# Optimization experiments

Hardware: AMD Instinct MI355X
Metric: run time of the kernel (lower is better)

## Reference

```python
import jax, jax.numpy as jnp
import numpy as np

B, C, H, W = 16, 1, 512, 512
D, F, KH, KW = 4, 24, 5, 5   # numWienerFilters, output_features, reg-filter size
BKH, BKW = 9, 9              # blur kernel size
LB, UB = 1e-4, 1e-2


def psf2otf(psf, shape):
    # zero-pad psf to `shape`, circularly shift its center to (0,0), FFT
    kh, kw = psf.shape[-2], psf.shape[-1]
    pad = [(0, 0)] * (psf.ndim - 2) + [(0, shape[0] - kh), (0, shape[1] - kw)]
    p = jnp.pad(psf, pad)
    p = jnp.roll(p, shift=(-((kh - 1) // 2), -((kw - 1) // 2)), axis=(-2, -1))
    return jnp.fft.fft2(p)


def _taper_profile(proj, n):
    # autocorrelation of the psf projection, periodized to length n (MATLAB edgetaper)
    z = jnp.zeros(n - 1, proj.dtype).at[: proj.shape[0]].set(proj)
    zf = jnp.fft.fft(z)
    acf = jnp.real(jnp.fft.ifft(zf * jnp.conj(zf)))
    acf = jnp.concatenate([acf, acf[:1]])
    return acf / acf.max()


def _normalize_weights(w, scale):
    # WeightNormalization5D: zero-mean + L2-normalize over (C,kh,kw), times scale
    w = w - w.mean(axis=(2, 3, 4), keepdims=True)
    nrm = jnp.sqrt(jnp.sum(w * w, axis=(2, 3, 4), keepdims=True))
    return w * (scale[..., None, None, None] / nrm)


def setup_inputs():
    key = jax.random.key(0)
    ks = jax.random.split(key, 4)
    x = jax.random.uniform(ks[0], (B, C, H, W), jnp.float32)
    bk = jax.random.uniform(ks[1], (BKH, BKW), jnp.float32) + 1e-3
    bk = bk / bk.sum()  # normalized blur PSF
    stdn = jax.random.uniform(ks[2], (B,), jnp.float32) * 0.1 + 0.01
    conv_weights = jax.random.normal(ks[3], (D, F, C, KH, KW), jnp.float32)
    scale = jnp.full((D, F), 0.1, jnp.float32)
    alpha = jnp.log(jnp.logspace(np.log10(LB), np.log10(UB), D))[:, None].astype(jnp.float32)
    return {"x": x, "blur_kernel": bk, "stdn": stdn,
            "conv_weights": conv_weights, "scale": scale, "alpha": alpha}


def reference(x, blur_kernel, stdn, conv_weights, scale, alpha):
    kh, kw = blur_kernel.shape
    # getPad2RetainShape
    pt, pb = (kh + 1) // 2 - 1, kh - (kh + 1) // 2
    pl, pr = (kw + 1) // 2 - 1, kw - (kw + 1) // 2
    xp = jnp.pad(x, ((0, 0), (0, 0), (pt, pb), (pl, pr)), mode="symmetric")
    Hp, Wp = xp.shape[-2], xp.shape[-1]
    otf = psf2otf(blur_kernel, (Hp, Wp))                     # (Hp,Wp) complex
    # EdgeTaper: blend image with its circular blur near borders
    br = _taper_profile(blur_kernel.sum(axis=1), Hp)
    bc = _taper_profile(blur_kernel.sum(axis=0), Wp)
    taper = (1.0 - br)[:, None] * (1.0 - bc)[None, :]
    blurred = jnp.real(jnp.fft.ifft2(jnp.fft.fft2(xp) * otf))
    xp = taper * xp + (1.0 - taper) * blurred
    # regularization-filter OTFs
    w = _normalize_weights(conv_weights, scale)              # (D,F,C,kh,kw)
    G = psf2otf(w, (Hp, Wp))                                 # (D,F,C,Hp,Wp)
    S = jnp.sum(G.real ** 2 + G.imag ** 2, axis=1)           # (D,C,Hp,Wp)
    a = jnp.exp(alpha)[:, :, None, None]                     # (D,1,1,1)
    B2 = otf.real ** 2 + otf.imag ** 2                       # (Hp,Wp)
    denom = B2[None, None] + a * S                           # (D,C,Hp,Wp)
    Y = jnp.conj(otf) * jnp.fft.fft2(xp)                     # (B,C,Hp,Wp)
    Xf = Y[:, None] / denom[None]                            # (B,D,C,Hp,Wp)
    out = jnp.real(jnp.fft.ifft2(Xf))[..., pt:Hp - pb, pl:Wp - pr]
    # colored-noise std factor per (wiener filter, channel)
    cvar = jnp.mean(B2[None, None] / denom ** 2, axis=(-2, -1))   # (D,C)
    cvar = jnp.broadcast_to(cvar[None], (x.shape[0],) + cvar.shape)  # (B,D,C)
    cstdn = jnp.sqrt(stdn[:, None] ** 2 * cvar.mean(axis=2))        # (B,D)
    return out, cstdn
```

## Files before the change

kernel.cpp:

```cpp
#include <hip/hip_runtime.h>
#include <math.h>

#define NP    520
#define NN    (520*520)
#define HH    512
#define NPIX  (512*512)
#define NB    16
#define NPAIR 8
#define ND    4
#define NF    24
#define KS    544
#define RS    576
#define PLANE ((size_t)RS*KS)
#define S8P   (8*PLANE)
#define E9SZ  (NP*9)
#define CSZ   (ND*9*NP)
#define NBORD 18396
#define PADCH 5536
#define TWO_PI 6.283185307179586f

typedef unsigned short u16;
typedef __attribute__((ext_vector_type(8))) short bf16x8;
typedef __attribute__((ext_vector_type(4))) float f32x4;

__device__ __forceinline__ int wrap520(int t){ t %= NP; return t < 0 ? t + NP : t; }

__device__ __forceinline__ u16 f2bf(float f){
  unsigned u = __float_as_uint(f);
  u += 0x7FFFu + ((u >> 16) & 1u);
  return (u16)(u >> 16);
}
__device__ __forceinline__ float bf2f(u16 h){
  return __uint_as_float(((unsigned)h) << 16);
}
__device__ __forceinline__ void gll16(const u16* g, u16* l){
  __builtin_amdgcn_global_load_lds(
      (const __attribute__((address_space(1))) void*)g,
      (__attribute__((address_space(3))) void*)l, 16, 0, 0);
}
template<int N> __device__ __forceinline__ void vmwait(){
  if constexpr (N == 0)       asm volatile("s_waitcnt vmcnt(0)" ::: "memory");
  else if constexpr (N == 4)  asm volatile("s_waitcnt vmcnt(4)" ::: "memory");
  else if constexpr (N == 6)  asm volatile("s_waitcnt vmcnt(6)" ::: "memory");
  else if constexpr (N == 8)  asm volatile("s_waitcnt vmcnt(8)" ::: "memory");
  else if constexpr (N == 12) asm volatile("s_waitcnt vmcnt(12)" ::: "memory");
}
#define MF(a,b,c) __builtin_amdgcn_mfma_f32_16x16x32_bf16((a),(b),(c),0,0,0)


__global__ __launch_bounds__(256) void zwb_k(u16* __restrict__ slabs, int nSlices,
                                             u16* __restrict__ wf, u16* __restrict__ wi){
  int idx = blockIdx.x*256 + threadIdx.x;
  int nA = nSlices*PADCH;
  if (idx < nA){
    int pl = idx / PADCH, cc = idx % PADCH;
    int row, col;
    if (cc < 1728){ row = cc/3; col = 520 + (cc%3)*8; }
    else { int c2 = cc - 1728; row = 520 + c2/68; col = (c2%68)*8; }
    bf16x8 z = {0,0,0,0,0,0,0,0};
    *(bf16x8*)(slabs + (size_t)pl*PLANE + (size_t)row*KS + col) = z;
    return;
  }
  idx -= nA;
  if (idx >= (int)PLANE) return;
  int r = idx / KS, k = idx % KS;
  float fr=0.f, fi=0.f, ir=0.f, ii=0.f;
  if (r < NP && k < NP){
    int m = (int)(((long long)r * (long long)k) % NP);
    float ang = TWO_PI * (float)m / (float)NP;
    float s, c; sincosf(ang, &s, &c);
    fr = c; fi = -s;
    ir = c * (1.0f/NP); ii = s * (1.0f/NP);
  }
  wf[0*PLANE+idx] = f2bf(fr); wf[1*PLANE+idx] = f2bf(fi);
  wi[0*PLANE+idx] = f2bf(ir); wi[1*PLANE+idx] = f2bf(ii);
}

__global__ __launch_bounds__(256) void setup1_k(const float* __restrict__ bk,
                                                const float* __restrict__ cw,
                                                const float* __restrict__ scale,
                                                float* __restrict__ e9,
                                                float* __restrict__ r_row, float* __restrict__ r_col,
                                                float* __restrict__ wn){
  int idx = blockIdx.x*256 + threadIdx.x;
  if (idx < NP*9){
    int u = idx / 9, t = idx % 9;
    int m = wrap520(u*(t-4));
    float ang = TWO_PI * (float)m / (float)NP;
    float s, c; sincosf(ang, &s, &c);
    e9[idx] = c; e9[E9SZ + idx] = -s;
    return;
  }
  idx -= NP*9;
  if (idx < 18){
    int k = idx % 9;
    bool rowp = (idx < 9);
    float proj[9];
    for (int m = 0; m < 9; ++m){
      float a = 0.f;
      for (int j = 0; j < 9; ++j) a += rowp ? bk[m*9+j] : bk[j*9+m];
      proj[m] = a;
    }
    float acc = 0.f;
    for (int m = 0; m + k < 9; ++m) acc += proj[m] * proj[m+k];
    (rowp ? r_row : r_col)[k] = acc;
    return;
  }
  idx -= 18;
  if (idx >= ND*NF) return;
  const float* wp = cw + idx*25;
  float mean = 0.f;
  for (int k = 0; k < 25; ++k) mean += wp[k];
  mean *= (1.0f/25.0f);
  float ss = 0.f;
  for (int k = 0; k < 25; ++k){ float d = wp[k]-mean; ss += d*d; }
  float sc = scale[idx] / sqrtf(ss);
  for (int k = 0; k < 25; ++k) wn[idx*25+k] = (wp[k]-mean)*sc;
}

__global__ __launch_bounds__(256) void setup2_k(const float* __restrict__ bk,
                                                const float* __restrict__ e9,
                                                const float* __restrict__ wn,
                                                float* __restrict__ T, float* __restrict__ R){
  int idx = blockIdx.x*256 + threadIdx.x;
  if (idx < 9*NP){
    int i = idx / NP, v = idx % NP;
    float tr = 0.f, ti = 0.f;
    #pragma unroll
    for (int j = 0; j < 9; ++j){
      float w = bk[i*9+j];
      tr += w * e9[v*9+j];
      ti += w * e9[E9SZ + v*9+j];
    }
    T[idx] = tr; T[9*NP + idx] = ti;
    return;
  }
  idx -= 9*NP;
  if (idx >= ND*81) return;
  int d = idx / 81, t = idx % 81;
  int di = t/9 - 4, dj = t%9 - 4;
  int i0 = di > 0 ? di : 0, i1 = di < 0 ? 4+di : 4;
  int j0 = dj > 0 ? dj : 0, j1 = dj < 0 ? 4+dj : 4;
  float acc = 0.f;
  for (int f = 0; f < NF; ++f){
    const float* w = wn + (d*NF+f)*25;
    for (int i = i0; i <= i1; ++i)
      for (int j = j0; j <= j1; ++j)
        acc += w[i*5+j] * w[(i-di)*5 + (j-dj)];
  }
  R[idx] = acc;
}

__global__ void C_k(const float* __restrict__ R, const float* __restrict__ e9,
                    float* __restrict__ Ctab){
  int idx = blockIdx.x*blockDim.x + threadIdx.x;
  if (idx >= ND*9*NP) return;
  int v = idx % NP, t9 = idx / NP;
  int d = t9 / 9, t = t9 % 9;
  float cr = 0.f, ci = 0.f;
  #pragma unroll
  for (int s = 0; s < 9; ++s){
    float r = R[d*81 + t*9 + s];
    cr += r * e9[v*9+s];
    ci += r * e9[E9SZ + v*9+s];
  }
  Ctab[idx] = cr; Ctab[CSZ + idx] = ci;
}

__global__ __launch_bounds__(256) void denomMT2_k(
    const float* __restrict__ Tb, const float* __restrict__ e9,
    const float* __restrict__ Ctab, const float* __restrict__ alpha,
    float* __restrict__ MTre, float* __restrict__ MTim, float* __restrict__ cvar){
  __shared__ float red[256];
  const int d = blockIdx.y;
  const int p = blockIdx.x*256 + threadIdx.x;
  float contrib = 0.f;
  if (p < NN){
    int u = p % NP, v = p / NP;
    float ar = 0.f, ai = 0.f;
    #pragma unroll
    for (int i = 0; i < 9; ++i){
      float er = e9[u*9+i], ei = e9[E9SZ + u*9+i];
      float tr = Tb[i*NP+v], ti = Tb[9*NP + i*NP+v];
      ar += er*tr - ei*ti;
      ai += er*ti + ei*tr;
    }
    float S = 0.f;
    #pragma unroll
    for (int t = 0; t < 9; ++t){
      float er = e9[u*9+t], ei = e9[E9SZ + u*9+t];
      float cr = Ctab[(d*9+t)*NP + v], ci = Ctab[CSZ + (d*9+t)*NP + v];
      S += er*cr - ei*ci;
    }
    float B2 = ar*ar + ai*ai;
    size_t idx = (size_t)d*NN + p;
    float dv = B2 + expf(alpha[d]) * S;
    MTre[idx] = ar / dv;
    MTim[idx] = -ai / dv;
    contrib = B2 / (dv*dv);
  }
  red[threadIdx.x] = contrib; __syncthreads();
  for (int s = 128; s > 0; s >>= 1){
    if (threadIdx.x < s) red[threadIdx.x] += red[threadIdx.x+s];
    __syncthreads();
  }
  if (threadIdx.x == 0) atomicAdd(&cvar[d], red[0]);
}

__global__ void cstdn_k(const float* __restrict__ stdn, const float* __restrict__ cvar,
                        float* __restrict__ out){
  int t = threadIdx.x;
  if (t >= NB*ND) return;
  int b = t >> 2, d = t & 3;
  float s = stdn[b];
  out[(size_t)NB*ND*NPIX + t] = sqrtf(s*s*cvar[d]*(1.0f/(float)NN));
}

__global__ __launch_bounds__(256) void pad_tr_k(const float* __restrict__ x,
                                                u16* __restrict__ MA){
  __shared__ float tile[64][65];
  const int q  = blockIdx.z;
  const int r0 = blockIdx.y * 64;
  const int c0 = blockIdx.x * 64;
  const int t  = threadIdx.x;
  const float* xq = x + (size_t)q*NPIX;
  const int jl = t & 63, ib = t >> 6;
  const bool fast = (c0 >= 64 && c0 <= 448 && r0 >= 64 && r0 <= 448);

  if (fast){
    #pragma unroll 1
    for (int pass = 0; pass < 16; ++pass){
      int il = ib + pass*4;
      tile[il][jl] = xq[(size_t)(c0+il-4)*HH + (r0+jl-4)];
    }
  } else {
    #pragma unroll 1
    for (int pass = 0; pass < 16; ++pass){
      int il = ib + pass*4;
      int I = c0 + il, J = r0 + jl;
      float v = 0.f;
      if (I < NP && J < NP){
        int si = I - 4; si = (si < 0) ? (-si-1) : ((si >= HH) ? (2*HH-1-si) : si);
        int sj = J - 4; sj = (sj < 0) ? (-sj-1) : ((sj >= HH) ? (2*HH-1-sj) : sj);
        v = xq[(size_t)si*HH + sj];
      }
      tile[il][jl] = v;
    }
  }
  __syncthreads();

  const int cchunk = t & 7, rb = t >> 3;
  const int pair = q >> 1, pl = q & 1;
  #pragma unroll
  for (int half = 0; half < 2; ++half){
    int rl = rb + half*32;
    int r = r0 + rl, cg = c0 + cchunk*8;
    if (r >= NP || cg >= NP) continue;
    bf16x8 vh;
    #pragma unroll
    for (int e = 0; e < 8; ++e)
      vh[e] = (short)f2bf(tile[cchunk*8+e][rl]);
    size_t o = (size_t)pair*PLANE + (size_t)r*KS + cg;
    *(bf16x8*)(MA + (size_t)pl*S8P + o) = vh;
  }
}

__global__ __launch_bounds__(256) void border_k(const float* __restrict__ x,
                                                const float* __restrict__ bk,
                                                const float* __restrict__ r_row,
                                                const float* __restrict__ r_col,
                                                u16* __restrict__ MA){
  __shared__ float bks[81], rr_[9], rc_[9];
  if (threadIdx.x < 81) bks[threadIdx.x] = bk[threadIdx.x];
  if (threadIdx.x < 9){ rr_[threadIdx.x] = r_row[threadIdx.x]; rc_[threadIdx.x] = r_col[threadIdx.x]; }
  __syncthreads();
  int idx = blockIdx.x*256 + threadIdx.x;
  if (idx >= NB*NBORD) return;
  int q = idx / NBORD, t = idx % NBORD;
  int I, J;
  if (t < 9360){ int ri = t / 520; I = (ri < 9) ? ri : 502 + ri; J = t % 520; }
  else { int s = t - 9360; I = 9 + s / 18; int ci = s % 18; J = (ci < 9) ? ci : 502 + ci; }
  const float* xq = x + (size_t)q*NPIX;
  auto XP = [&](int ii, int jj)->float{
    int si = ii - 4; si = (si < 0) ? (-si-1) : ((si >= HH) ? (2*HH-1-si) : si);
    int sj = jj - 4; sj = (sj < 0) ? (-sj-1) : ((sj >= HH) ? (2*HH-1-sj) : sj);
    return xq[(size_t)si*HH + sj];
  };
  float v = XP(I, J);
  float brv = (I < 9) ? rr_[I] : ((I >= 511) ? rr_[519-I] : 0.f);
  float bcv = (J < 9) ? rc_[J] : ((J >= 511) ? rc_[519-J] : 0.f);
  brv /= rr_[0]; bcv /= rc_[0];
  float tp = (1.f - brv) * (1.f - bcv);
  float blur = 0.f;
  for (int a = 0; a < 9; ++a){
    int ii = wrap520(I - a + 4);
    for (int b2 = 0; b2 < 9; ++b2){
      int jj = wrap520(J - b2 + 4);
      blur += bks[a*9+b2] * XP(ii, jj);
    }
  }
  v = tp*v + (1.f - tp)*blur;
  int pair = q >> 1, pl = q & 1;
  MA[(size_t)pl*S8P + (size_t)pair*PLANE + (size_t)J*KS + I] = f2bf(v);
}

__global__ __launch_bounds__(256) void maskF_k(const u16* __restrict__ IN, u16* __restrict__ OUT,
                                               const float* __restrict__ Mre, const float* __restrict__ Mim){
  int idx = blockIdx.x*256 + threadIdx.x;
  if (idx >= NPAIR*NP*65) return;
  int pr = idx / (NP*65), rem = idx % (NP*65);
  int r = rem / 65, c0 = (rem % 65)*8;
  size_t o = (size_t)pr*PLANE + (size_t)r*KS + c0;
  bf16x8 qr = *(const bf16x8*)(IN + 0*S8P + o);
  bf16x8 qi = *(const bf16x8*)(IN + 1*S8P + o);
  const float* mrp = Mre + (size_t)r*NP + c0;
  const float* mip = Mim + (size_t)r*NP + c0;
  bf16x8 o0, o1;
  #pragma unroll
  for (int e = 0; e < 8; ++e){
    float vr = bf2f((u16)qr[e]), vi = bf2f((u16)qi[e]);
    float mr = mrp[e], mi = mip[e];
    o0[e] = (short)f2bf(vr*mr - vi*mi);
    o1[e] = (short)f2bf(vr*mi + vi*mr);
  }
  *(bf16x8*)(OUT + 0*S8P + o) = o0;
  *(bf16x8*)(OUT + 1*S8P + o) = o1;
}

template<int BM, int CROP, int MASKOUT>
__global__ __launch_bounds__(256) void gemm_k(
    const u16* __restrict__ P, size_t pPl, size_t pZp, size_t pZd,
    const u16* __restrict__ Q, size_t qPl, size_t qZp, size_t qZd,
    u16* __restrict__ O, size_t oPl, size_t oZp, size_t oZd,
    float* __restrict__ cropOut, int dBase,
    const float* __restrict__ Mre, const float* __restrict__ Mim)
{
  constexpr int NW = 4;
  constexpr int FR = BM/32;
  constexpr int TR = BM/16;
  constexpr int LPW = 4*TR/NW;
  constexpr int PLSTR = BM*32;
  constexpr int BUF = 4*PLSTR;
  constexpr int NK = KS/32;
  __shared__ u16 lds[3*BUF];
  const int tid = threadIdx.x;
  const int l = tid & 63, w = tid >> 6;

  const int gx = gridDim.x, gy = gridDim.y;
  int lin = blockIdx.x + gx*(blockIdx.y + gy*blockIdx.z);
  int ntot = gx*gy*gridDim.z;
  int q8 = ntot >> 3, r8 = ntot & 7;
  int xcd = lin & 7, id8 = lin >> 3;
  int nl = (xcd < r8 ? xcd*(q8+1) : r8*(q8+1) + (xcd-r8)*q8) + id8;
  int BX = nl % gx; int t2 = nl / gx;
  int BY = t2 % gy; int BZ = t2 / gy;

  const int pair = BZ & 7;
  const int dd = dBase + (BZ >> 3);
  const int R0 = BY * BM, C0 = BX * BM;

  const u16* Pb = P + (size_t)pair*pZp + (size_t)dd*pZd;
  const u16* Qb = Q + (size_t)pair*qZp + (size_t)dd*qZd;

  const int s = l >> 2;
  const int cs8 = ((l & 3) ^ ((s >> 1) & 3)) * 8;
  const size_t pOff0 = (size_t)(R0 + s)*KS + cs8;
  const size_t qOff0 = (size_t)(C0 + s)*KS + cs8;

  const int lm = l & 15, lc = l >> 4;
  const int wm = w >> 1, wn = w & 1;

  f32x4 zero4 = {0.f, 0.f, 0.f, 0.f};
  f32x4 aRe[FR][FR], aIm[FR][FR];
  #pragma unroll
  for (int i = 0; i < FR; ++i)
    #pragma unroll
    for (int j = 0; j < FR; ++j){ aRe[i][j] = zero4; aIm[i][j] = zero4; }

  auto STAGE = [&](int bi, int k0){
    u16* dst = lds + bi*BUF;
    #pragma unroll
    for (int i = 0; i < LPW; ++i){
      int t = w + i*NW;
      int q2 = t / TR, r2 = t % TR;
      const u16* src = (q2 < 2) ? (Pb + (size_t)q2*pPl + pOff0)
                                : (Qb + (size_t)(q2-2)*qPl + qOff0);
      gll16(src + (size_t)(r2*16)*KS + k0, dst + q2*PLSTR + r2*512);
    }
  };

  STAGE(0, 0);
  STAGE(1, 32);

  #pragma unroll 1
  for (int kt = 0; kt < NK; ++kt){
    if (kt + 2 < NK) STAGE((kt+2)%3, (kt+2)*32);
    if (kt + 2 < NK)      vmwait<2*LPW>();
    else if (kt + 1 < NK) vmwait<LPW>();
    else                  vmwait<0>();
    __builtin_amdgcn_sched_barrier(0);
    __builtin_amdgcn_s_barrier();
    __builtin_amdgcn_sched_barrier(0);

    const u16* buf = lds + (kt%3)*BUF;
    bf16x8 pf[FR][2];
    #pragma unroll
    for (int mi = 0; mi < FR; ++mi){
      int r = wm*(FR*16) + mi*16 + lm;
      int co = ((lc ^ ((r >> 1) & 3)) << 3);
      pf[mi][0] = *(const bf16x8*)(buf + 0*PLSTR + r*32 + co);
      pf[mi][1] = *(const bf16x8*)(buf + 1*PLSTR + r*32 + co);
    }
    #pragma unroll
    for (int ni = 0; ni < FR; ++ni){
      int r = wn*(FR*16) + ni*16 + lm;
      int co = ((lc ^ ((r >> 1) & 3)) << 3);
      bf16x8 q0 = *(const bf16x8*)(buf + 2*PLSTR + r*32 + co);
      bf16x8 q1 = *(const bf16x8*)(buf + 3*PLSTR + r*32 + co);
      #pragma unroll
      for (int mi = 0; mi < FR; ++mi){
        bf16x8 nw = pf[mi][1] ^ (short)0x8000;
        f32x4 re = aRe[mi][ni], im = aIm[mi][ni];
        re = MF(pf[mi][0], q0, re);
        re = MF(nw,        q1, re);
        im = MF(pf[mi][0], q1, im);
        im = MF(pf[mi][1], q0, im);
        aRe[mi][ni] = re; aIm[mi][ni] = im;
      }
    }
    __builtin_amdgcn_sched_barrier(0);
    __builtin_amdgcn_s_barrier();
    __builtin_amdgcn_sched_barrier(0);
  }

  u16* Ob = O ? (O + (size_t)pair*oZp + (size_t)dd*oZd) : nullptr;
  #pragma unroll
  for (int mi = 0; mi < FR; ++mi)
    #pragma unroll
    for (int ni = 0; ni < FR; ++ni){
      int cb = C0 + wn*(FR*16) + ni*16 + lm;
      int rb = R0 + wm*(FR*16) + mi*16 + lc*4;
      #pragma unroll
      for (int e = 0; e < 4; ++e){
        int rr = rb + e;
        float vr = aRe[mi][ni][e], vi = aIm[mi][ni][e];
        if (CROP){
          if (rr >= 4 && rr < 516 && cb >= 4 && cb < 516){
            size_t px = (size_t)(rr-4)*HH + (cb-4);
            cropOut[((size_t)(2*pair  )*ND + dd)*NPIX + px] = vr;
            cropOut[((size_t)(2*pair+1)*ND + dd)*NPIX + px] = vi;
          }
        } else if (MASKOUT){
          if (rr < NP && cb < NP){
            size_t o = (size_t)rr*KS + cb;
            size_t mo = (size_t)rr*NP + cb;
            #pragma unroll
            for (int d2 = 0; d2 < ND; ++d2){
              float mr = Mre[(size_t)d2*NN + mo], mi2 = Mim[(size_t)d2*NN + mo];
              u16* Od = O + (size_t)d2*oZd + (size_t)pair*oZp;
              Od[0*oPl+o] = f2bf(vr*mr - vi*mi2);
              Od[1*oPl+o] = f2bf(vr*mi2 + vi*mr);
            }
          }
        } else {
          if (rr < NP && cb < NP){
            size_t o = (size_t)rr*KS + cb;
            Ob[0*oPl+o] = f2bf(vr);
            Ob[1*oPl+o] = f2bf(vi);
          }
        }
      }
    }
}


extern "C" void kernel_launch(void* const* d_in, const int* in_sizes, int n_in,
                              void* d_out, int out_size, void* d_ws, size_t ws_size,
                              hipStream_t stream){
  const float* x     = (const float*)d_in[0];
  const float* bk    = (const float*)d_in[1];
  const float* stdn  = (const float*)d_in[2];
  const float* cw    = (const float*)d_in[3];
  const float* scale = (const float*)d_in[4];
  const float* alpha = (const float*)d_in[5];
  float* out = (float*)d_out;

  char* base = (char*)d_ws;
  const size_t UNIT = 16*PLANE*sizeof(u16);
  size_t off;
  auto alloc = [&](size_t bytes)->void*{
    void* p = base + off;
    off += (bytes + 255) & ~(size_t)255;
    return p;
  };

  u16 *MA, *MB, *MC, *Dm, *Do, *WF, *WI;
  float *MTre, *MTim, *e9, *Tb, *Rarr, *Ctab, *r_row, *r_col, *wn, *cvar;
  auto layout = [&](bool bigL){
    off = 0;
    MA = (u16*)alloc(UNIT);
    MB = (u16*)alloc(UNIT);
    if (bigL){ Dm = (u16*)alloc(4*UNIT); Do = (u16*)alloc(4*UNIT); MC = nullptr; }
    else     { MC = (u16*)alloc(UNIT);   Dm = nullptr; Do = nullptr; }
    WF = (u16*)alloc(2*PLANE*sizeof(u16));
    WI = (u16*)alloc(2*PLANE*sizeof(u16));
    MTre = (float*)alloc((size_t)ND*NN*4);
    MTim = (float*)alloc((size_t)ND*NN*4);
    e9   = (float*)alloc(2*E9SZ*4);
    Tb   = (float*)alloc(2*9*NP*4);
    Rarr = (float*)alloc(ND*81*4);
    Ctab = (float*)alloc(2*CSZ*4);
    r_row = (float*)alloc(64);
    r_col = (float*)alloc(64);
    wn   = (float*)alloc(ND*NF*25*4);
    cvar = (float*)alloc(64);
    return off;
  };
  bool big = (layout(true) <= ws_size);
  if (!big){
    if (layout(false) > ws_size) return;
  }

  hipMemsetAsync(cvar, 0, ND*sizeof(float), stream);

  const int nSlices = big ? 160 : 48;
  {
    int ztot = nSlices*PADCH + (int)PLANE;
    zwb_k<<<(ztot+255)/256, 256, 0, stream>>>(MA, nSlices, WF, WI);
  }
  setup1_k<<<(NP*9+18+ND*NF+255)/256, 256, 0, stream>>>(bk, cw, scale, e9, r_row, r_col, wn);
  setup2_k<<<(9*NP+ND*81+255)/256, 256, 0, stream>>>(bk, e9, wn, Tb, Rarr);
  C_k     <<<(ND*9*NP+255)/256, 256, 0, stream>>>(Rarr, e9, Ctab);
  {
    dim3 gd((NN+255)/256, ND);
    denomMT2_k<<<gd, 256, 0, stream>>>(Tb, e9, Ctab, alpha, MTre, MTim, cvar);
  }
  cstdn_k <<<1, 64, 0, stream>>>(stdn, cvar, out);
  pad_tr_k<<<dim3(9, 9, NB), 256, 0, stream>>>(x, MA);
  border_k<<<(NB*NBORD+255)/256, 256, 0, stream>>>(x, bk, r_row, r_col, MA);

  gemm_k<64,0,0><<<dim3(9,9,8),256,0,stream>>>(
      WF, PLANE, 0, 0,   MA, S8P, PLANE, 0,   MB, S8P, PLANE, 0,
      nullptr, 0, nullptr, nullptr);

  if (big){
    gemm_k<64,0,1><<<dim3(9,9,8),256,0,stream>>>(
        WF, PLANE, 0, 0,   MB, S8P, PLANE, 0,   Dm, S8P, PLANE, 16*PLANE,
        nullptr, 0, MTre, MTim);
    gemm_k<96,0,0><<<dim3(6,6,32),256,0,stream>>>(
        WI, PLANE, 0, 0,   Dm, S8P, PLANE, 16*PLANE,   Do, S8P, PLANE, 16*PLANE,
        nullptr, 0, nullptr, nullptr);
    gemm_k<96,1,0><<<dim3(6,6,32),256,0,stream>>>(
        Do, S8P, PLANE, 16*PLANE,   WI, PLANE, 0, 0,   nullptr, 0, 0, 0,
        out, 0, nullptr, nullptr);
  } else {
    gemm_k<64,0,0><<<dim3(9,9,8),256,0,stream>>>(
        WF, PLANE, 0, 0,   MB, S8P, PLANE, 0,   MC, S8P, PLANE, 0,
        nullptr, 0, nullptr, nullptr);
    const int mgrid = (NPAIR*NP*65 + 255)/256;
    for (int d = 0; d < ND; ++d){
      maskF_k<<<mgrid,256,0,stream>>>(MC, MA, MTre + (size_t)d*NN, MTim + (size_t)d*NN);
      gemm_k<96,0,0><<<dim3(6,6,8),256,0,stream>>>(
          WI, PLANE, 0, 0,   MA, S8P, PLANE, 0,   MB, S8P, PLANE, 0,
          nullptr, 0, nullptr, nullptr);
      gemm_k<96,1,0><<<dim3(6,6,8),256,0,stream>>>(
          MB, S8P, PLANE, 0,   WI, PLANE, 0, 0,   nullptr, 0, 0, 0,
          out, d, nullptr, nullptr);
    }
  }
}
```

Before: 328.8 us.

## Restructure GEMM pipeline, merge denominator D-loop, shrink zero-padding work

Result: no change. 325.4 us (-1.0%).

```diff
diff --git a/kernel.cpp b/kernel.cpp
--- a/kernel.cpp
+++ b/kernel.cpp
@@ -48,10 +48,10 @@
 #define MF(a,b,c) __builtin_amdgcn_mfma_f32_16x16x32_bf16((a),(b),(c),0,0,0)
 
 
-__global__ __launch_bounds__(256) void zwb_k(u16* __restrict__ slabs, int nSlices,
+__global__ __launch_bounds__(256) void zwb_k(u16* __restrict__ slabs,
                                              u16* __restrict__ wf, u16* __restrict__ wi){
   int idx = blockIdx.x*256 + threadIdx.x;
-  int nA = nSlices*PADCH;
+  const int nA = 16*PADCH;
   if (idx < nA){
     int pl = idx / PADCH, cc = idx % PADCH;
     int row, col;
@@ -172,39 +172,42 @@
     const float* __restrict__ Ctab, const float* __restrict__ alpha,
     float* __restrict__ MTre, float* __restrict__ MTim, float* __restrict__ cvar){
   __shared__ float red[256];
-  const int d = blockIdx.y;
   const int p = blockIdx.x*256 + threadIdx.x;
-  float contrib = 0.f;
+  float contrib[ND] = {0.f, 0.f, 0.f, 0.f};
   if (p < NN){
     int u = p % NP, v = p / NP;
+    float er9[9], ei9[9];
+    #pragma unroll
+    for (int i = 0; i < 9; ++i){ er9[i] = e9[u*9+i]; ei9[i] = e9[E9SZ + u*9+i]; }
     float ar = 0.f, ai = 0.f;
     #pragma unroll
     for (int i = 0; i < 9; ++i){
-      float er = e9[u*9+i], ei = e9[E9SZ + u*9+i];
       float tr = Tb[i*NP+v], ti = Tb[9*NP + i*NP+v];
-      ar += er*tr - ei*ti;
-      ai += er*ti + ei*tr;
-    }
-    float S = 0.f;
-    #pragma unroll
-    for (int t = 0; t < 9; ++t){
-      float er = e9[u*9+t], ei = e9[E9SZ + u*9+t];
-      float cr = Ctab[(d*9+t)*NP + v], ci = Ctab[CSZ + (d*9+t)*NP + v];
-      S += er*cr - ei*ci;
+      ar += er9[i]*tr - ei9[i]*ti;
+      ai += er9[i]*ti + ei9[i]*tr;
     }
     float B2 = ar*ar + ai*ai;
-    size_t idx = (size_t)d*NN + p;
-    float dv = B2 + expf(alpha[d]) * S;
-    MTre[idx] = ar / dv;
-    MTim[idx] = -ai / dv;
-    contrib = B2 / (dv*dv);
-  }
-  red[threadIdx.x] = contrib; __syncthreads();
-  for (int s = 128; s > 0; s >>= 1){
-    if (threadIdx.x < s) red[threadIdx.x] += red[threadIdx.x+s];
+    #pragma unroll
+    for (int d = 0; d < ND; ++d){
+      float S = 0.f;
+      #pragma unroll
+      for (int t = 0; t < 9; ++t)
+        S += er9[t]*Ctab[(d*9+t)*NP + v] - ei9[t]*Ctab[CSZ + (d*9+t)*NP + v];
+      float dv = B2 + expf(alpha[d]) * S;
+      MTre[(size_t)d*NN + p] = ar / dv;
+      MTim[(size_t)d*NN + p] = -ai / dv;
+      contrib[d] = B2 / (dv*dv);
+    }
+  }
+  for (int d = 0; d < ND; ++d){
+    red[threadIdx.x] = contrib[d]; __syncthreads();
+    for (int s = 128; s > 0; s >>= 1){
+      if (threadIdx.x < s) red[threadIdx.x] += red[threadIdx.x+s];
+      __syncthreads();
+    }
+    if (threadIdx.x == 0) atomicAdd(&cvar[d], red[0]);
     __syncthreads();
   }
-  if (threadIdx.x == 0) atomicAdd(&cvar[d], red[0]);
 }
 
 __global__ void cstdn_k(const float* __restrict__ stdn, const float* __restrict__ cvar,
@@ -394,13 +397,11 @@
 
   #pragma unroll 1
   for (int kt = 0; kt < NK; ++kt){
-    if (kt + 2 < NK) STAGE((kt+2)%3, (kt+2)*32);
-    if (kt + 2 < NK)      vmwait<2*LPW>();
-    else if (kt + 1 < NK) vmwait<LPW>();
-    else                  vmwait<0>();
+    if (kt + 1 < NK) vmwait<LPW>(); else vmwait<0>();
     __builtin_amdgcn_sched_barrier(0);
     __builtin_amdgcn_s_barrier();
     __builtin_amdgcn_sched_barrier(0);
+    if (kt + 2 < NK) STAGE((kt+2)%3, (kt+2)*32);
 
     const u16* buf = lds + (kt%3)*BUF;
     bf16x8 pf[FR][2];
@@ -411,12 +412,20 @@
       pf[mi][0] = *(const bf16x8*)(buf + 0*PLSTR + r*32 + co);
       pf[mi][1] = *(const bf16x8*)(buf + 1*PLSTR + r*32 + co);
     }
+    int rq0 = wn*(FR*16) + lm;
+    int cq0 = ((lc ^ ((rq0 >> 1) & 3)) << 3);
+    bf16x8 q0 = *(const bf16x8*)(buf + 2*PLSTR + rq0*32 + cq0);
+    bf16x8 q1 = *(const bf16x8*)(buf + 3*PLSTR + rq0*32 + cq0);
     #pragma unroll
     for (int ni = 0; ni < FR; ++ni){
-      int r = wn*(FR*16) + ni*16 + lm;
-      int co = ((lc ^ ((r >> 1) & 3)) << 3);
-      bf16x8 q0 = *(const bf16x8*)(buf + 2*PLSTR + r*32 + co);
-      bf16x8 q1 = *(const bf16x8*)(buf + 3*PLSTR + r*32 + co);
+      bf16x8 nq0 = q0, nq1 = q1;
+      if (ni + 1 < FR){
+        int r = wn*(FR*16) + (ni+1)*16 + lm;
+        int co = ((lc ^ ((r >> 1) & 3)) << 3);
+        nq0 = *(const bf16x8*)(buf + 2*PLSTR + r*32 + co);
+        nq1 = *(const bf16x8*)(buf + 3*PLSTR + r*32 + co);
+      }
+      __builtin_amdgcn_s_setprio(1);
       #pragma unroll
       for (int mi = 0; mi < FR; ++mi){
         bf16x8 nw = pf[mi][1] ^ (short)0x8000;
@@ -427,10 +436,9 @@
         im = MF(pf[mi][1], q0, im);
         aRe[mi][ni] = re; aIm[mi][ni] = im;
       }
-    }
-    __builtin_amdgcn_sched_barrier(0);
-    __builtin_amdgcn_s_barrier();
-    __builtin_amdgcn_sched_barrier(0);
+      __builtin_amdgcn_s_setprio(0);
+      q0 = nq0; q1 = nq1;
+    }
   }
 
   u16* Ob = O ? (O + (size_t)pair*oZp + (size_t)dd*oZd) : nullptr;
@@ -451,9 +459,9 @@
             cropOut[((size_t)(2*pair+1)*ND + dd)*NPIX + px] = vi;
           }
         } else if (MASKOUT){
-          if (rr < NP && cb < NP){
+          if (cb < KS){
             size_t o = (size_t)rr*KS + cb;
-            size_t mo = (size_t)rr*NP + cb;
+            size_t mo = (size_t)(rr < NP ? rr : 0)*NP + (cb < NP ? cb : 0);
             #pragma unroll
             for (int d2 = 0; d2 < ND; ++d2){
               float mr = Mre[(size_t)d2*NN + mo], mi2 = Mim[(size_t)d2*NN + mo];
@@ -463,7 +471,7 @@
             }
           }
         } else {
-          if (rr < NP && cb < NP){
+          if (cb < KS){
             size_t o = (size_t)rr*KS + cb;
             Ob[0*oPl+o] = f2bf(vr);
             Ob[1*oPl+o] = f2bf(vi);
@@ -523,18 +531,14 @@
 
   hipMemsetAsync(cvar, 0, ND*sizeof(float), stream);
 
-  const int nSlices = big ? 160 : 48;
   {
-    int ztot = nSlices*PADCH + (int)PLANE;
-    zwb_k<<<(ztot+255)/256, 256, 0, stream>>>(MA, nSlices, WF, WI);
+    int ztot = 16*PADCH + (int)PLANE;
+    zwb_k<<<(ztot+255)/256, 256, 0, stream>>>(MA, WF, WI);
   }
   setup1_k<<<(NP*9+18+ND*NF+255)/256, 256, 0, stream>>>(bk, cw, scale, e9, r_row, r_col, wn);
   setup2_k<<<(9*NP+ND*81+255)/256, 256, 0, stream>>>(bk, e9, wn, Tb, Rarr);
   C_k     <<<(ND*9*NP+255)/256, 256, 0, stream>>>(Rarr, e9, Ctab);
-  {
-    dim3 gd((NN+255)/256, ND);
-    denomMT2_k<<<gd, 256, 0, stream>>>(Tb, e9, Ctab, alpha, MTre, MTim, cvar);
-  }
+  denomMT2_k<<<(NN+255)/256, 256, 0, stream>>>(Tb, e9, Ctab, alpha, MTre, MTim, cvar);
   cstdn_k <<<1, 64, 0, stream>>>(stdn, cvar, out);
   pad_tr_k<<<dim3(9, 9, NB), 256, 0, stream>>>(x, MA);
   border_k<<<(NB*NBORD+255)/256, 256, 0, stream>>>(x, bk, r_row, r_col, MA);
```
